# Kernel optimization log

Hardware: AMD Instinct MI355X
Metric: run time of the kernel (lower is better)

## Reference

```python
import jax, jax.numpy as jnp
import numpy as np

B, T, DIM = 2, 1024, 1024
H, DH, E, K = 8, 64, 5, 3
SCALE = DH ** -0.5


def topk_mask(scores, k):
    # 0/1 mask of the top-k entries along the last (expert) axis
    _, idx = jax.lax.top_k(scores, k)          # [..., k]
    return jax.nn.one_hot(idx, scores.shape[-1], dtype=scores.dtype).sum(-2)


def setup_inputs() -> dict:
    key = jax.random.key(0)
    ks = jax.random.split(key, 7)
    s = DIM ** -0.5
    x = jax.random.normal(ks[0], (B, T, DIM), jnp.float32)
    Wq = jax.random.normal(ks[1], (DIM, H * DH), jnp.float32) * s
    Wk = jax.random.normal(ks[2], (DIM, H * DH), jnp.float32) * s
    Wv = jax.random.normal(ks[3], (DIM, H * E * DH), jnp.float32) * s
    Ws = jax.random.normal(ks[4], (DIM, H * E), jnp.float32) * s
    Wd = jax.random.normal(ks[5], (DIM, H * E), jnp.float32) * s
    # grouped conv weight: per head h, expert e: map dim_head -> dim
    Wo = jax.random.normal(ks[6], (H, E, DIM, DH), jnp.float32) * (DH ** -0.5)
    causal_mask = jnp.triu(jnp.ones((T, T), bool), 1)[None, None]  # [1,1,T,T]
    return {"x": x, "Wq": Wq, "Wk": Wk, "Wv": Wv, "Ws": Ws, "Wd": Wd,
            "Wo": Wo, "causal_mask": causal_mask}


def reference(x, Wq, Wk, Wv, Ws, Wd, Wo, causal_mask):
    # source-side routing scores (soft: gate values kept on top-k)
    ss = jax.nn.sigmoid((x @ Ws).reshape(B, T, H, E))
    ss = ss * topk_mask(ss, K)
    # destination-side routing (hard 0/1 top-k mask)
    sd = topk_mask(jax.nn.sigmoid((x @ Wd).reshape(B, T, H, E)), K)

    q = (x @ Wq).reshape(B, T, H, DH).transpose(0, 2, 1, 3)  # [B,H,T,DH]
    k = (x @ Wk).reshape(B, T, H, DH).transpose(0, 2, 1, 3)
    v_exp = (x @ Wv).reshape(B, T, H, E, DH)                  # per-expert V
    v = jnp.einsum('bthe,bthed->bhtd', ss, v_exp)             # routed V mix

    scores = jnp.einsum('bhid,bhjd->bhij', q * SCALE, k)
    scores = jnp.where(causal_mask, -1e9, scores)
    probs = jax.nn.softmax(scores, axis=-1)
    o = jnp.einsum('bhij,bhjd->bhid', probs, v)               # [B,H,T,DH]

    # expert output projection (h,e: DH -> DIM), gated by sd, summed over h,e
    out = jnp.einsum('bthe,bhtc,hedc->btd', sd, o, Wo)        # [B,T,DIM]
    return out
```

## Files before the change

kernel.cpp:

```cpp
#include <hip/hip_runtime.h>

typedef unsigned short u16;
typedef __bf16 bf16x8 __attribute__((ext_vector_type(8)));
typedef float floatx4 __attribute__((ext_vector_type(4)));

#define B_   2
#define T_   1024
#define DIM_ 1024
#define H_   8
#define DH_  64
#define E_   5

#define N1   3584
#define M_   2048
#define KOUT 2560

__device__ __forceinline__ u16 f2bf(float f) {
  union { float f; unsigned u; } v; v.f = f;
  unsigned r = v.u + 0x7FFFu + ((v.u >> 16) & 1u);
  return (u16)(r >> 16);
}
__device__ __forceinline__ float bf2f(u16 h) {
  union { unsigned u; float f; } v; v.u = ((unsigned)h) << 16;
  return v.f;
}

__device__ __forceinline__ void async_cp16(const void* g, void* l) {
  __builtin_amdgcn_global_load_lds(
      (const __attribute__((address_space(1))) unsigned int*)g,
      (__attribute__((address_space(3))) unsigned int*)l, 16, 0, 0);
}


__global__ __launch_bounds__(256)
void transpose_all_kernel(const float* __restrict__ Wq, const float* __restrict__ Wk,
                          const float* __restrict__ Wv, u16* __restrict__ WT) {
  __shared__ float tile[32][33];
  int k0 = blockIdx.x * 32;
  int nt = blockIdx.y;
  const float* W; int N, n0, nofs;
  if (nt < 16)      { W = Wq; N = 512;  n0 = nt * 32;        nofs = 0; }
  else if (nt < 32) { W = Wk; N = 512;  n0 = (nt - 16) * 32; nofs = 512; }
  else              { W = Wv; N = 2560; n0 = (nt - 32) * 32; nofs = 1024; }
  int tx = threadIdx.x & 31, ty = threadIdx.x >> 5;
  #pragma unroll
  for (int i = 0; i < 32; i += 8)
    tile[ty + i][tx] = W[(size_t)(k0 + ty + i) * N + n0 + tx];
  __syncthreads();
  #pragma unroll
  for (int i = 0; i < 32; i += 8)
    WT[(size_t)(nofs + n0 + ty + i) * 1024 + k0 + tx] = f2bf(tile[tx][ty + i]);
}

__global__ void build_WoT_kernel(const float* __restrict__ Wo, u16* __restrict__ WoT) {
  int i = blockIdx.x * 256 + threadIdx.x;
  int c4 = i & 15;
  int t  = i >> 4;
  int d  = t / 40;
  int he = t - d * 40;
  float4 v = *(const float4*)(Wo + ((size_t)(he * 1024 + d) * 64 + c4 * 4));
  union { u16 s[4]; uint2 u; } o;
  o.s[0] = f2bf(v.x); o.s[1] = f2bf(v.y); o.s[2] = f2bf(v.z); o.s[3] = f2bf(v.w);
  *(uint2*)(WoT + (size_t)d * KOUT + he * 64 + c4 * 4) = o.u;
}


__global__ __launch_bounds__(256)
void logits_kernel(const float* __restrict__ x, const float* __restrict__ Ws,
                   const float* __restrict__ Wd, float* __restrict__ Pl,
                   u16* __restrict__ xb) {
  __shared__ float xs[16][68];
  __shared__ float wt[16][80];
  const int tid = threadIdx.x;
  const int m0 = blockIdx.x * 64;
  const int kbeg = blockIdx.y * 128;
  const int tx = tid & 15, ty = tid >> 4;
  const int srow = tid >> 2, skq = tid & 3;

  float acc[4][5];
  #pragma unroll
  for (int r = 0; r < 4; ++r)
    #pragma unroll
    for (int c = 0; c < 5; ++c) acc[r][c] = 0.f;

  for (int s = 0; s < 8; ++s) {
    const int k0 = kbeg + s * 16;
    __syncthreads();
    {
      float4 v = *(const float4*)(x + (size_t)(m0 + srow) * 1024 + k0 + skq * 4);
      xs[skq * 4 + 0][srow] = v.x; xs[skq * 4 + 1][srow] = v.y;
      xs[skq * 4 + 2][srow] = v.z; xs[skq * 4 + 3][srow] = v.w;
      union { u16 h[4]; uint2 u; } o;
      o.h[0] = f2bf(v.x); o.h[1] = f2bf(v.y); o.h[2] = f2bf(v.z); o.h[3] = f2bf(v.w);
      *(uint2*)(xb + (size_t)(m0 + srow) * 1024 + k0 + skq * 4) = o.u;
    }
    #pragma unroll
    for (int j = 0; j < 5; ++j) {
      int f = j * 256 + tid;
      int kk = f / 80, c = f - kk * 80;
      wt[kk][c] = (c < 40) ? Ws[(size_t)(k0 + kk) * 40 + c]
                           : Wd[(size_t)(k0 + kk) * 40 + c - 40];
    }
    __syncthreads();

    #pragma unroll
    for (int kk = 0; kk < 16; ++kk) {
      float4 xv = *(const float4*)(&xs[kk][ty * 4]);
      float xr[4] = {xv.x, xv.y, xv.z, xv.w};
      #pragma unroll
      for (int c = 0; c < 5; ++c) {
        float wv = wt[kk][tx * 5 + c];
        #pragma unroll
        for (int r = 0; r < 4; ++r) acc[r][c] = fmaf(xr[r], wv, acc[r][c]);
      }
    }
  }

  float* P = Pl + (size_t)blockIdx.y * M_ * 80;
  #pragma unroll
  for (int r = 0; r < 4; ++r)
    #pragma unroll
    for (int c = 0; c < 5; ++c)
      P[(size_t)(m0 + ty * 4 + r) * 80 + tx * 5 + c] = acc[r][c];
}

__global__ __launch_bounds__(256)
void topk_kernel(const float* __restrict__ Pl, float* __restrict__ ssg,
                 float* __restrict__ sdg) {
  __shared__ float lg[16][80];
  const int bt0 = blockIdx.x * 16;
  const int tid = threadIdx.x;
  #pragma unroll
  for (int j = 0; j < 5; ++j) {
    int f = j * 256 + tid;
    int r = f / 80, c = f - r * 80;
    float s = 0.f;
    #pragma unroll
    for (int z = 0; z < 8; ++z)
      s += Pl[(size_t)z * M_ * 80 + (size_t)(bt0 + r) * 80 + c];
    lg[r][c] = s;
  }
  __syncthreads();

  const int r = tid >> 4, h = (tid >> 1) & 7, side = tid & 1;
  float z[E_], g[E_]; bool sel[E_];
  #pragma unroll
  for (int e = 0; e < E_; ++e) {
    z[e] = lg[r][side * 40 + h * E_ + e];
    g[e] = 1.f / (1.f + __expf(-z[e]));
    sel[e] = false;
  }
  #pragma unroll
  for (int it = 0; it < 3; ++it) {
    int bi = 0; float bv = -3e38f;
    #pragma unroll
    for (int e = 0; e < E_; ++e)
      if (!sel[e] && z[e] > bv) { bv = z[e]; bi = e; }
    sel[bi] = true;
  }
  float* dst = (side == 0) ? ssg : sdg;
  #pragma unroll
  for (int e = 0; e < E_; ++e)
    dst[(size_t)(bt0 + r) * 40 + h * E_ + e] =
        (side == 0) ? (sel[e] ? g[e] : 0.f) : (sel[e] ? 1.f : 0.f);
}


template <int SPLITK>
__global__ __launch_bounds__(256)
void gemm4w_kernel(const u16* __restrict__ A, const u16* __restrict__ Bm,
                   u16* __restrict__ C, int N, int Kd) {
  constexpr int BK = 32;
  __shared__ __align__(16) u16 As[128 * BK];
  __shared__ __align__(16) u16 Bs[128 * BK];
  const int tid = threadIdx.x;
  const int w = tid >> 6, lane = tid & 63;
  const int ln15 = lane & 15, quad = lane >> 4;
  const int wm = w >> 1, wn = w & 1;
  const int bm0 = blockIdx.x * 128, bn0 = blockIdx.y * 128;
  const int lrow = lane >> 2;
  const int lg8 = (((lane & 3) ^ ((lane >> 3) & 3))) * 8;
  const int swz = (ln15 >> 1) & 3;
  const int kchunk = Kd / SPLITK;
  const int kbeg = blockIdx.z * kchunk;

  floatx4 acc[4][4];
  #pragma unroll
  for (int i = 0; i < 4; ++i)
    #pragma unroll
    for (int j = 0; j < 4; ++j) acc[i][j] = (floatx4){0.f, 0.f, 0.f, 0.f};

  for (int k0 = kbeg; k0 < kbeg + kchunk; k0 += BK) {
    __syncthreads();
    #pragma unroll
    for (int j = 0; j < 2; ++j) {
      int i = w * 2 + j;
      async_cp16(A + (size_t)(bm0 + i * 16 + lrow) * Kd + k0 + lg8, (char*)As + i * 1024);
      async_cp16(Bm + (size_t)(bn0 + i * 16 + lrow) * Kd + k0 + lg8, (char*)Bs + i * 1024);
    }
    __builtin_amdgcn_s_waitcnt(0);
    __syncthreads();

    bf16x8 af[4], bf[4];
    #pragma unroll
    for (int mt = 0; mt < 4; ++mt)
      af[mt] = *(const bf16x8*)(As + (wm * 64 + mt * 16 + ln15) * BK + ((quad ^ swz) * 8));
    #pragma unroll
    for (int nt = 0; nt < 4; ++nt)
      bf[nt] = *(const bf16x8*)(Bs + (wn * 64 + nt * 16 + ln15) * BK + ((quad ^ swz) * 8));
    #pragma unroll
    for (int mt = 0; mt < 4; ++mt)
      #pragma unroll
      for (int nt = 0; nt < 4; ++nt)
        acc[mt][nt] = __builtin_amdgcn_mfma_f32_16x16x32_bf16(af[mt], bf[nt], acc[mt][nt], 0, 0, 0);
  }

  u16* Cz = C + (size_t)blockIdx.z * M_ * N;
  #pragma unroll
  for (int mt = 0; mt < 4; ++mt)
    #pragma unroll
    for (int nt = 0; nt < 4; ++nt)
      #pragma unroll
      for (int r = 0; r < 4; ++r) {
        int m = bm0 + wm * 64 + mt * 16 + quad * 4 + r;
        int n = bn0 + wn * 64 + nt * 16 + ln15;
        Cz[(size_t)m * N + n] = f2bf(acc[mt][nt][r]);
      }
}

__global__ void reduce4_kernel(const u16* __restrict__ Pk, float* __restrict__ out) {
  int i = blockIdx.x * 256 + threadIdx.x;
  size_t base = (size_t)i * 8;
  float s[8] = {0.f, 0.f, 0.f, 0.f, 0.f, 0.f, 0.f, 0.f};
  #pragma unroll
  for (int z = 0; z < 4; ++z) {
    union { uint4 v; u16 h[8]; } u;
    u.v = *(const uint4*)(Pk + (size_t)z * M_ * 1024 + base);
    #pragma unroll
    for (int c = 0; c < 8; ++c) s[c] += bf2f(u.h[c]);
  }
  float4 o0 = {s[0], s[1], s[2], s[3]}, o1 = {s[4], s[5], s[6], s[7]};
  *(float4*)(out + base) = o0;
  *(float4*)(out + base + 4) = o1;
}


__global__ __launch_bounds__(256)
void vmix_tr_kernel(const u16* __restrict__ c1, const float* __restrict__ ssg,
                    u16* __restrict__ vT) {
  __shared__ u16 tile[32][33];
  const int bh = blockIdx.x;
  const int b = bh >> 3, h = bh & 7;
  const int t0 = blockIdx.y * 32, d0 = blockIdx.z * 32;
  const int dh = threadIdx.x & 31, tl = threadIdx.x >> 5;
  #pragma unroll
  for (int i = 0; i < 4; ++i) {
    int trow = tl + i * 8;
    size_t bt = (size_t)b * T_ + t0 + trow;
    const u16* ve = c1 + bt * N1 + 1024 + h * (E_ * 64) + d0 + dh;
    const float* g = ssg + bt * 40 + h * E_;
    float s = 0.f;
    #pragma unroll
    for (int e = 0; e < E_; ++e) s = fmaf(g[e], bf2f(ve[e * 64]), s);
    tile[trow][dh] = f2bf(s);
  }
  __syncthreads();
  #pragma unroll
  for (int i = 0; i < 4; ++i) {
    int d = d0 + tl + i * 8;
    vT[((size_t)(b * H_ + h) * DH_ + d) * T_ + t0 + dh] = tile[dh][tl + i * 8];
  }
}


__global__ __launch_bounds__(256)
void attn_kernel(const u16* __restrict__ c1, const u16* __restrict__ vT,
                 const float* __restrict__ sdg, u16* __restrict__ Ab) {
  __shared__ __align__(16) u16 Qs[32 * 64];
  __shared__ __align__(16) u16 Ks[2][64 * 64];
  __shared__ __align__(16) u16 Vs[2][64 * 64];
  __shared__ __align__(16) u16 Ps[2][32 * 72];
  __shared__ float Om[2][32][68];
  __shared__ float Ml[2][32], Ll[2][32];
  const int qi = blockIdx.x;
  const int bh = blockIdx.y;
  const int b = bh >> 3, h = bh & 7;
  const int tid = threadIdx.x;
  const int w = tid >> 6, lane = tid & 63;
  const int ln15 = lane & 15, quad = lane >> 4;
  const int hh = w >> 1, wq = w & 1;
  const int q0 = qi * 32;
  const int nkt = (qi >> 1) + 1;
  const int h0n = (nkt + 1) >> 1;
  const int r8 = lane >> 3;
  const int g8 = ((lane & 7) ^ ((lane >> 3) & 7)) * 8;
  const int swz = ln15 & 7;

  async_cp16(c1 + (size_t)(b * T_ + q0 + w * 8 + r8) * N1 + h * DH_ + g8,
             (char*)Qs + w * 1024);

  floatx4 O[4];
  float m_st[4], l_st[4];
  #pragma unroll
  for (int j = 0; j < 4; ++j) {
    O[j] = (floatx4){0.f, 0.f, 0.f, 0.f};
    m_st[j] = -3e38f; l_st[j] = 0.f;
  }
  const int qrow = q0 + wq * 16 + quad * 4;

  for (int j = 0; j < h0n; ++j) {
    const int myt = hh ? (h0n + j) : j;
    const bool act = (hh == 0) || (h0n + j < nkt);
    __syncthreads();
    if (w < 2 || h0n + j < nkt) {
      const int tk = (w < 2 ? j : h0n + j) * 64;
      if ((w & 1) == 0) {
        #pragma unroll
        for (int i = 0; i < 8; ++i)
          async_cp16(c1 + (size_t)(b * T_ + tk + i * 8 + r8) * N1 + 512 + h * DH_ + g8,
                     (char*)Ks[w >> 1] + i * 1024);
      } else {
        #pragma unroll
        for (int i = 0; i < 8; ++i)
          async_cp16(vT + (size_t)((b * H_ + h) * DH_ + i * 8 + r8) * T_ + tk + g8,
                     (char*)Vs[w >> 1] + i * 1024);
      }
    }
    __builtin_amdgcn_s_waitcnt(0);
    __syncthreads();

    float p[4][4];
    if (act) {
      const int tk0 = myt * 64;
      floatx4 S[4];
      #pragma unroll
      for (int nt = 0; nt < 4; ++nt) S[nt] = (floatx4){0.f, 0.f, 0.f, 0.f};
      #pragma unroll
      for (int ks = 0; ks < 2; ++ks) {
        bf16x8 a = *(const bf16x8*)(Qs + (wq * 16 + ln15) * 64 + (((ks * 4 + quad) ^ swz)) * 8);
        #pragma unroll
        for (int nt = 0; nt < 4; ++nt) {
          bf16x8 bv = *(const bf16x8*)(&Ks[hh][(nt * 16 + ln15) * 64 + (((ks * 4 + quad) ^ swz)) * 8]);
          S[nt] = __builtin_amdgcn_mfma_f32_16x16x32_bf16(a, bv, S[nt], 0, 0, 0);
        }
      }
      float rmax[4], alpha[4], rsum[4];
      #pragma unroll
      for (int r = 0; r < 4; ++r) rmax[r] = -3e38f;
      #pragma unroll
      for (int nt = 0; nt < 4; ++nt) {
        int col = tk0 + nt * 16 + ln15;
        #pragma unroll
        for (int r = 0; r < 4; ++r) {
          float s = S[nt][r] * 0.125f;
          if (col > qrow + r) s = -3e38f;
          p[nt][r] = s;
          rmax[r] = fmaxf(rmax[r], s);
        }
      }
      #pragma unroll
      for (int r = 0; r < 4; ++r) {
        #pragma unroll
        for (int off = 1; off < 16; off <<= 1)
          rmax[r] = fmaxf(rmax[r], __shfl_xor(rmax[r], off));
        float mn = fmaxf(m_st[r], rmax[r]);
        alpha[r] = __expf(m_st[r] - mn);
        m_st[r] = mn;
        rsum[r] = 0.f;
      }
      #pragma unroll
      for (int nt = 0; nt < 4; ++nt)
        #pragma unroll
        for (int r = 0; r < 4; ++r) {
          float e = __expf(p[nt][r] - m_st[r]);
          p[nt][r] = e;
          rsum[r] += e;
        }
      #pragma unroll
      for (int r = 0; r < 4; ++r) {
        #pragma unroll
        for (int off = 1; off < 16; off <<= 1)
          rsum[r] += __shfl_xor(rsum[r], off);
        l_st[r] = l_st[r] * alpha[r] + rsum[r];
      }
      #pragma unroll
      for (int nt = 0; nt < 4; ++nt)
        #pragma unroll
        for (int r = 0; r < 4; ++r) O[nt][r] *= alpha[r];
      #pragma unroll
      for (int nt = 0; nt < 4; ++nt)
        #pragma unroll
        for (int r = 0; r < 4; ++r)
          Ps[hh][(wq * 16 + quad * 4 + r) * 72 + nt * 16 + ln15] = f2bf(p[nt][r]);
    }
    __syncthreads();
    if (act) {
      #pragma unroll
      for (int ks = 0; ks < 2; ++ks) {
        bf16x8 a = *(const bf16x8*)(&Ps[hh][(wq * 16 + ln15) * 72 + ks * 32 + quad * 8]);
        #pragma unroll
        for (int nt = 0; nt < 4; ++nt) {
          bf16x8 bv = *(const bf16x8*)(&Vs[hh][(nt * 16 + ln15) * 64 + (((ks * 4 + quad) ^ swz)) * 8]);
          O[nt] = __builtin_amdgcn_mfma_f32_16x16x32_bf16(a, bv, O[nt], 0, 0, 0);
        }
      }
    }
  }

  #pragma unroll
  for (int nt = 0; nt < 4; ++nt)
    #pragma unroll
    for (int r = 0; r < 4; ++r)
      Om[hh][wq * 16 + quad * 4 + r][nt * 16 + ln15] = O[nt][r];
  if (ln15 == 0) {
    #pragma unroll
    for (int r = 0; r < 4; ++r) {
      Ml[hh][wq * 16 + quad * 4 + r] = m_st[r];
      Ll[hh][wq * 16 + quad * 4 + r] = l_st[r];
    }
  }
  __syncthreads();

  const int rr = tid >> 3, cg = (tid & 7) * 8;
  float m0 = Ml[0][rr], m1 = Ml[1][rr];
  float l0 = Ll[0][rr], l1 = Ll[1][rr];
  float m = fmaxf(m0, m1);
  float a0 = __expf(m0 - m), a1 = __expf(m1 - m);
  float inv = 1.f / (l0 * a0 + l1 * a1);
  float oc[8];
  #pragma unroll
  for (int cc = 0; cc < 8; ++cc)
    oc[cc] = (Om[0][rr][cg + cc] * a0 + Om[1][rr][cg + cc] * a1) * inv;
  size_t bt = (size_t)b * T_ + q0 + rr;
  #pragma unroll
  for (int e = 0; e < E_; ++e) {
    float g = sdg[bt * 40 + h * E_ + e];
    union { u16 s[8]; uint4 v; } o;
    #pragma unroll
    for (int cc = 0; cc < 8; ++cc) o.s[cc] = f2bf(g * oc[cc]);
    *(uint4*)(Ab + bt * KOUT + (h * E_ + e) * 64 + cg) = o.v;
  }
}


extern "C" void kernel_launch(void* const* d_in, const int* in_sizes, int n_in,
                              void* d_out, int out_size, void* d_ws, size_t ws_size,
                              hipStream_t stream) {
  const float* x  = (const float*)d_in[0];
  const float* Wq = (const float*)d_in[1];
  const float* Wk = (const float*)d_in[2];
  const float* Wv = (const float*)d_in[3];
  const float* Ws = (const float*)d_in[4];
  const float* Wd = (const float*)d_in[5];
  const float* Wo = (const float*)d_in[6];
  float* out = (float*)d_out;

  char* ws = (char*)d_ws;
  u16*   WoT  = (u16*)(ws + 0);
  u16*   xb   = (u16*)(ws + 5242880);
  u16*   WT   = (u16*)(ws + 9437184);
  u16*   c1   = (u16*)(ws + 16777216);
  float* ssg  = (float*)(ws + 31457280);
  float* sdg  = (float*)(ws + 31784960);
  u16*   vT   = (u16*)(ws + 32112640);
  u16*   Ab   = (u16*)(ws + 34209792);
  u16*   Pk   = (u16*)(ws + 46137344);
  float* Pl   = (float*)(ws + 62914560);

  logits_kernel<<<dim3(32, 8), 256, 0, stream>>>(x, Ws, Wd, Pl, xb);
  topk_kernel<<<128, 256, 0, stream>>>(Pl, ssg, sdg);

  transpose_all_kernel<<<dim3(32, 112), 256, 0, stream>>>(Wq, Wk, Wv, WT);
  build_WoT_kernel<<<2560, 256, 0, stream>>>(Wo, WoT);

  gemm4w_kernel<1><<<dim3(16, 28, 1), 256, 0, stream>>>(xb, WT, c1, N1, 1024);

  vmix_tr_kernel<<<dim3(16, 32, 2), 256, 0, stream>>>(c1, ssg, vT);

  attn_kernel<<<dim3(32, 16), 256, 0, stream>>>(c1, vT, sdg, Ab);

  gemm4w_kernel<4><<<dim3(16, 8, 4), 256, 0, stream>>>(Ab, WoT, Pk, 1024, KOUT);
  reduce4_kernel<<<1024, 256, 0, stream>>>(Pk, out);
}
```

Before: 192.5 us.

## Fuse sd gating into output GEMM, merge weight prep kernels, reorder attention blocks

Attention now writes a single per-head output [B,H,T,64] instead of five gated copies. The output-projection GEMM reads that buffer directly and zeroes A fragments using a packed 40-bit sd bitmask per token. This removes the large expanded Ab buffer and its write and read traffic. The two weight-conversion kernels are merged into one launch, and attention blocks are interleaved long/short causal tiles to balance load.

```diff
diff --git a/kernel.cpp b/kernel.cpp
--- a/kernel.cpp
+++ b/kernel.cpp
@@ -1,6 +1,7 @@
 #include <hip/hip_runtime.h>
 
 typedef unsigned short u16;
+typedef unsigned long long u64;
 typedef __bf16 bf16x8 __attribute__((ext_vector_type(8)));
 typedef float floatx4 __attribute__((ext_vector_type(4)));
 
@@ -33,35 +34,37 @@
 
 
 __global__ __launch_bounds__(256)
-void transpose_all_kernel(const float* __restrict__ Wq, const float* __restrict__ Wk,
-                          const float* __restrict__ Wv, u16* __restrict__ WT) {
+void prep_kernel(const float* __restrict__ Wq, const float* __restrict__ Wk,
+                 const float* __restrict__ Wv, const float* __restrict__ Wo,
+                 u16* __restrict__ WT, u16* __restrict__ WoT) {
   __shared__ float tile[32][33];
-  int k0 = blockIdx.x * 32;
-  int nt = blockIdx.y;
-  const float* W; int N, n0, nofs;
-  if (nt < 16)      { W = Wq; N = 512;  n0 = nt * 32;        nofs = 0; }
-  else if (nt < 32) { W = Wk; N = 512;  n0 = (nt - 16) * 32; nofs = 512; }
-  else              { W = Wv; N = 2560; n0 = (nt - 32) * 32; nofs = 1024; }
-  int tx = threadIdx.x & 31, ty = threadIdx.x >> 5;
-  #pragma unroll
-  for (int i = 0; i < 32; i += 8)
-    tile[ty + i][tx] = W[(size_t)(k0 + ty + i) * N + n0 + tx];
-  __syncthreads();
-  #pragma unroll
-  for (int i = 0; i < 32; i += 8)
-    WT[(size_t)(nofs + n0 + ty + i) * 1024 + k0 + tx] = f2bf(tile[tx][ty + i]);
-}
-
-__global__ void build_WoT_kernel(const float* __restrict__ Wo, u16* __restrict__ WoT) {
-  int i = blockIdx.x * 256 + threadIdx.x;
-  int c4 = i & 15;
-  int t  = i >> 4;
-  int d  = t / 40;
-  int he = t - d * 40;
-  float4 v = *(const float4*)(Wo + ((size_t)(he * 1024 + d) * 64 + c4 * 4));
-  union { u16 s[4]; uint2 u; } o;
-  o.s[0] = f2bf(v.x); o.s[1] = f2bf(v.y); o.s[2] = f2bf(v.z); o.s[3] = f2bf(v.w);
-  *(uint2*)(WoT + (size_t)d * KOUT + he * 64 + c4 * 4) = o.u;
+  if (blockIdx.y < 112) {
+    int k0 = blockIdx.x * 32;
+    int nt = blockIdx.y;
+    const float* W; int N, n0, nofs;
+    if (nt < 16)      { W = Wq; N = 512;  n0 = nt * 32;        nofs = 0; }
+    else if (nt < 32) { W = Wk; N = 512;  n0 = (nt - 16) * 32; nofs = 512; }
+    else              { W = Wv; N = 2560; n0 = (nt - 32) * 32; nofs = 1024; }
+    int tx = threadIdx.x & 31, ty = threadIdx.x >> 5;
+    #pragma unroll
+    for (int i = 0; i < 32; i += 8)
+      tile[ty + i][tx] = W[(size_t)(k0 + ty + i) * N + n0 + tx];
+    __syncthreads();
+    #pragma unroll
+    for (int i = 0; i < 32; i += 8)
+      WT[(size_t)(nofs + n0 + ty + i) * 1024 + k0 + tx] = f2bf(tile[tx][ty + i]);
+  } else {
+    int id = (blockIdx.y - 112) * 32 + blockIdx.x;
+    int i = id * 256 + threadIdx.x;
+    int c4 = i & 15;
+    int t  = i >> 4;
+    int d  = t / 40;
+    int he = t - d * 40;
+    float4 v = *(const float4*)(Wo + ((size_t)(he * 1024 + d) * 64 + c4 * 4));
+    union { u16 s[4]; uint2 u; } o;
+    o.s[0] = f2bf(v.x); o.s[1] = f2bf(v.y); o.s[2] = f2bf(v.z); o.s[3] = f2bf(v.w);
+    *(uint2*)(WoT + (size_t)d * KOUT + he * 64 + c4 * 4) = o.u;
+  }
 }
 
 
@@ -126,8 +129,9 @@
 
 __global__ __launch_bounds__(256)
 void topk_kernel(const float* __restrict__ Pl, float* __restrict__ ssg,
-                 float* __restrict__ sdg) {
+                 u64* __restrict__ sdb) {
   __shared__ float lg[16][80];
+  __shared__ unsigned char mb[16][8];
   const int bt0 = blockIdx.x * 16;
   const int tid = threadIdx.x;
   #pragma unroll
@@ -158,15 +162,26 @@
       if (!sel[e] && z[e] > bv) { bv = z[e]; bi = e; }
     sel[bi] = true;
   }
-  float* dst = (side == 0) ? ssg : sdg;
-  #pragma unroll
-  for (int e = 0; e < E_; ++e)
-    dst[(size_t)(bt0 + r) * 40 + h * E_ + e] =
-        (side == 0) ? (sel[e] ? g[e] : 0.f) : (sel[e] ? 1.f : 0.f);
-}
-
-
-template <int SPLITK>
+  if (side == 0) {
+    #pragma unroll
+    for (int e = 0; e < E_; ++e)
+      ssg[(size_t)(bt0 + r) * 40 + h * E_ + e] = sel[e] ? g[e] : 0.f;
+  } else {
+    unsigned bits = 0;
+    #pragma unroll
+    for (int e = 0; e < E_; ++e) bits |= (sel[e] ? 1u : 0u) << e;
+    mb[r][h] = (unsigned char)bits;
+  }
+  __syncthreads();
+  if (tid < 16) {
+    u64 m = 0;
+    #pragma unroll
+    for (int hh = 0; hh < 8; ++hh) m |= (u64)mb[tid][hh] << (5 * hh);
+    sdb[bt0 + tid] = m;
+  }
+}
+
+
 __global__ __launch_bounds__(256)
 void gemm4w_kernel(const u16* __restrict__ A, const u16* __restrict__ Bm,
                    u16* __restrict__ C, int N, int Kd) {
@@ -181,8 +196,6 @@
   const int lrow = lane >> 2;
   const int lg8 = (((lane & 3) ^ ((lane >> 3) & 3))) * 8;
   const int swz = (ln15 >> 1) & 3;
-  const int kchunk = Kd / SPLITK;
-  const int kbeg = blockIdx.z * kchunk;
 
   floatx4 acc[4][4];
   #pragma unroll
@@ -190,7 +203,7 @@
     #pragma unroll
     for (int j = 0; j < 4; ++j) acc[i][j] = (floatx4){0.f, 0.f, 0.f, 0.f};
 
-  for (int k0 = kbeg; k0 < kbeg + kchunk; k0 += BK) {
+  for (int k0 = 0; k0 < Kd; k0 += BK) {
     __syncthreads();
     #pragma unroll
     for (int j = 0; j < 2; ++j) {
@@ -215,7 +228,6 @@
         acc[mt][nt] = __builtin_amdgcn_mfma_f32_16x16x32_bf16(af[mt], bf[nt], acc[mt][nt], 0, 0, 0);
   }
 
-  u16* Cz = C + (size_t)blockIdx.z * M_ * N;
   #pragma unroll
   for (int mt = 0; mt < 4; ++mt)
     #pragma unroll
@@ -224,7 +236,82 @@
       for (int r = 0; r < 4; ++r) {
         int m = bm0 + wm * 64 + mt * 16 + quad * 4 + r;
         int n = bn0 + wn * 64 + nt * 16 + ln15;
-        Cz[(size_t)m * N + n] = f2bf(acc[mt][nt][r]);
+        C[(size_t)m * N + n] = f2bf(acc[mt][nt][r]);
+      }
+}
+
+
+__global__ __launch_bounds__(256)
+void gemm2f_kernel(const u16* __restrict__ o_bh, const u16* __restrict__ WoT,
+                   const u64* __restrict__ sdb, u16* __restrict__ Pk) {
+  constexpr int BK = 32, Kd = KOUT;
+  __shared__ __align__(16) u16 As[128 * BK];
+  __shared__ __align__(16) u16 Bs[128 * BK];
+  const int tid = threadIdx.x;
+  const int w = tid >> 6, lane = tid & 63;
+  const int ln15 = lane & 15, quad = lane >> 4;
+  const int wm = w >> 1, wn = w & 1;
+  const int bm0 = blockIdx.x * 128, bn0 = blockIdx.y * 128;
+  const int b = bm0 >> 10;
+  const int t_base = bm0 & 1023;
+  const int lrow = lane >> 2;
+  const int lg8 = (((lane & 3) ^ ((lane >> 3) & 3))) * 8;
+  const int swz = (ln15 >> 1) & 3;
+  const int kbeg = blockIdx.z * 640;
+
+  u64 sdr[4];
+  #pragma unroll
+  for (int mt = 0; mt < 4; ++mt)
+    sdr[mt] = sdb[bm0 + wm * 64 + mt * 16 + ln15];
+
+  floatx4 acc[4][4];
+  #pragma unroll
+  for (int i = 0; i < 4; ++i)
+    #pragma unroll
+    for (int j = 0; j < 4; ++j) acc[i][j] = (floatx4){0.f, 0.f, 0.f, 0.f};
+
+  for (int k0 = kbeg; k0 < kbeg + 640; k0 += BK) {
+    const int he = k0 >> 6;
+    const int h = (he * 205) >> 10;
+    const int c0 = k0 & 63;
+    const u16* abase = o_bh + ((size_t)((b * 8 + h) * 1024 + t_base) * 64) + c0;
+    __syncthreads();
+    #pragma unroll
+    for (int j = 0; j < 2; ++j) {
+      int i = w * 2 + j;
+      async_cp16(abase + (size_t)(i * 16 + lrow) * 64 + lg8, (char*)As + i * 1024);
+      async_cp16(WoT + (size_t)(bn0 + i * 16 + lrow) * Kd + k0 + lg8, (char*)Bs + i * 1024);
+    }
+    __builtin_amdgcn_s_waitcnt(0);
+    __syncthreads();
+
+    bf16x8 af[4], bf[4];
+    union { uint4 u; bf16x8 v; } z8; z8.u = (uint4){0u, 0u, 0u, 0u};
+    #pragma unroll
+    for (int mt = 0; mt < 4; ++mt) {
+      af[mt] = *(const bf16x8*)(As + (wm * 64 + mt * 16 + ln15) * BK + ((quad ^ swz) * 8));
+      if (!((sdr[mt] >> he) & 1)) af[mt] = z8.v;
+    }
+    #pragma unroll
+    for (int nt = 0; nt < 4; ++nt)
+      bf[nt] = *(const bf16x8*)(Bs + (wn * 64 + nt * 16 + ln15) * BK + ((quad ^ swz) * 8));
+    #pragma unroll
+    for (int mt = 0; mt < 4; ++mt)
+      #pragma unroll
+      for (int nt = 0; nt < 4; ++nt)
+        acc[mt][nt] = __builtin_amdgcn_mfma_f32_16x16x32_bf16(af[mt], bf[nt], acc[mt][nt], 0, 0, 0);
+  }
+
+  u16* Cz = Pk + (size_t)blockIdx.z * M_ * 1024;
+  #pragma unroll
+  for (int mt = 0; mt < 4; ++mt)
+    #pragma unroll
+    for (int nt = 0; nt < 4; ++nt)
+      #pragma unroll
+      for (int r = 0; r < 4; ++r) {
+        int m = bm0 + wm * 64 + mt * 16 + quad * 4 + r;
+        int n = bn0 + wn * 64 + nt * 16 + ln15;
+        Cz[(size_t)m * 1024 + n] = f2bf(acc[mt][nt][r]);
       }
 }
 
@@ -275,14 +362,15 @@
 
 __global__ __launch_bounds__(256)
 void attn_kernel(const u16* __restrict__ c1, const u16* __restrict__ vT,
-                 const float* __restrict__ sdg, u16* __restrict__ Ab) {
+                 u16* __restrict__ o_bh) {
   __shared__ __align__(16) u16 Qs[32 * 64];
   __shared__ __align__(16) u16 Ks[2][64 * 64];
   __shared__ __align__(16) u16 Vs[2][64 * 64];
   __shared__ __align__(16) u16 Ps[2][32 * 72];
   __shared__ float Om[2][32][68];
   __shared__ float Ml[2][32], Ll[2][32];
-  const int qi = blockIdx.x;
+  const int bx = blockIdx.x;
+  const int qi = (bx & 1) ? (bx >> 1) : (31 - (bx >> 1));
   const int bh = blockIdx.y;
   const int b = bh >> 3, h = bh & 7;
   const int tid = threadIdx.x;
@@ -427,19 +515,11 @@
   float m = fmaxf(m0, m1);
   float a0 = __expf(m0 - m), a1 = __expf(m1 - m);
   float inv = 1.f / (l0 * a0 + l1 * a1);
-  float oc[8];
+  union { u16 s[8]; uint4 v; } o;
   #pragma unroll
   for (int cc = 0; cc < 8; ++cc)
-    oc[cc] = (Om[0][rr][cg + cc] * a0 + Om[1][rr][cg + cc] * a1) * inv;
-  size_t bt = (size_t)b * T_ + q0 + rr;
-  #pragma unroll
-  for (int e = 0; e < E_; ++e) {
-    float g = sdg[bt * 40 + h * E_ + e];
-    union { u16 s[8]; uint4 v; } o;
-    #pragma unroll
-    for (int cc = 0; cc < 8; ++cc) o.s[cc] = f2bf(g * oc[cc]);
-    *(uint4*)(Ab + bt * KOUT + (h * E_ + e) * 64 + cg) = o.v;
-  }
+    o.s[cc] = f2bf((Om[0][rr][cg + cc] * a0 + Om[1][rr][cg + cc] * a1) * inv);
+  *(uint4*)(o_bh + ((size_t)((b * 8 + h) * 1024 + q0 + rr)) * 64 + cg) = o.v;
 }
 
 
@@ -461,24 +541,23 @@
   u16*   WT   = (u16*)(ws + 9437184);
   u16*   c1   = (u16*)(ws + 16777216);
   float* ssg  = (float*)(ws + 31457280);
-  float* sdg  = (float*)(ws + 31784960);
-  u16*   vT   = (u16*)(ws + 32112640);
-  u16*   Ab   = (u16*)(ws + 34209792);
-  u16*   Pk   = (u16*)(ws + 46137344);
-  float* Pl   = (float*)(ws + 62914560);
+  u64*   sdb  = (u64*)(ws + 31784960);
+  u16*   o_bh = (u16*)(ws + 31801344);
+  u16*   vT   = (u16*)(ws + 33898496);
+  u16*   Pk   = (u16*)(ws + 35995648);
+  float* Pl   = (float*)(ws + 52772864);
 
   logits_kernel<<<dim3(32, 8), 256, 0, stream>>>(x, Ws, Wd, Pl, xb);
-  topk_kernel<<<128, 256, 0, stream>>>(Pl, ssg, sdg);
-
-  transpose_all_kernel<<<dim3(32, 112), 256, 0, stream>>>(Wq, Wk, Wv, WT);
-  build_WoT_kernel<<<2560, 256, 0, stream>>>(Wo, WoT);
-
-  gemm4w_kernel<1><<<dim3(16, 28, 1), 256, 0, stream>>>(xb, WT, c1, N1, 1024);
+  topk_kernel<<<128, 256, 0, stream>>>(Pl, ssg, sdb);
+
+  prep_kernel<<<dim3(32, 192), 256, 0, stream>>>(Wq, Wk, Wv, Wo, WT, WoT);
+
+  gemm4w_kernel<<<dim3(16, 28), 256, 0, stream>>>(xb, WT, c1, N1, 1024);
 
   vmix_tr_kernel<<<dim3(16, 32, 2), 256, 0, stream>>>(c1, ssg, vT);
 
-  attn_kernel<<<dim3(32, 16), 256, 0, stream>>>(c1, vT, sdg, Ab);
-
-  gemm4w_kernel<4><<<dim3(16, 8, 4), 256, 0, stream>>>(Ab, WoT, Pk, 1024, KOUT);
+  attn_kernel<<<dim3(32, 16), 256, 0, stream>>>(c1, vT, o_bh);
+
+  gemm2f_kernel<<<dim3(16, 8, 4), 256, 0, stream>>>(o_bh, WoT, sdb, Pk);
   reduce4_kernel<<<1024, 256, 0, stream>>>(Pk, out);
 }
```

Result: faster. 186.9 us (-2.9%).
